# Optimization experiments

Measured on AMD Instinct MI355X. Metric: run time of the kernel, lower is better.

Reference implementation:

```python
import jax, jax.numpy as jnp
import numpy as np

NUM_CODES = 8192
LATENT_DIM = 512
COMMITMENT_WEIGHT = 0.25


def l2_normalize(x, axis=-1, eps=1e-12):
    n = jnp.linalg.norm(x, axis=axis, keepdims=True)
    return x / jnp.maximum(n, eps)


def setup_inputs() -> dict:
    key = jax.random.key(0)
    k1, k2 = jax.random.split(key)
    z_e = jax.random.normal(k1, (32768, LATENT_DIM), dtype=jnp.float32)
    embeddings = jax.random.normal(k2, (NUM_CODES, LATENT_DIM), dtype=jnp.float32)
    return {"z_e": z_e, "embeddings": embeddings}


def reference(z_e, embeddings):
    B = z_e.shape[0]
    z_e_norm = l2_normalize(z_e, axis=-1)          # (B, D)
    emb_norm = l2_normalize(embeddings, axis=-1)   # (K, D)
    sim = z_e_norm @ emb_norm.T                    # (B, K) cosine similarity
    indices = jnp.argmax(sim, axis=-1)             # (B,)
    z_q = emb_norm[indices]                        # (B, D) gather

    commitment_loss = COMMITMENT_WEIGHT * jnp.mean(
        (z_e_norm - jax.lax.stop_gradient(z_q)) ** 2)
    codebook_loss = jnp.mean((jax.lax.stop_gradient(z_e_norm) - z_q) ** 2)

    # straight-through estimator
    z_q_ste = z_e_norm + jax.lax.stop_gradient(z_q - z_e_norm)

    # usage stats (one-hot mean via scatter-add)
    counts = jnp.zeros((NUM_CODES,), dtype=jnp.float32).at[indices].add(1.0)
    avg_probs = counts / B
    perplexity = jnp.exp(-jnp.sum(avg_probs * jnp.log(avg_probs + 1e-10)))
    utilization = jnp.mean((avg_probs > 0).astype(jnp.float32))

    return (z_q_ste, indices, commitment_loss, codebook_loss, perplexity,
            utilization)
```

## Files before the change

kernel.cpp:

```cpp
#include <hip/hip_runtime.h>

#define BROWS  32768
#define DDIM   512
#define NCODES 8192
#define NCHUNK 4
#define CHUNKN (NCODES / NCHUNK)
#define NSPLIT2 16
#define CHUNK2 (NCODES / NSPLIT2)
#define TM     128
#define TN     128
#define BK     32
#define NKT    (DDIM / BK)
#define MARGIN1 1.0e-3f
#define MARGIN  6e-6f

typedef unsigned short ushort_t;
typedef unsigned int   uint_t;
typedef unsigned long long ull_t;
typedef __attribute__((ext_vector_type(8))) short  short8;
typedef __attribute__((ext_vector_type(4))) float  floatx4;

__device__ __forceinline__ float wave_sum(float v) {
#pragma unroll
  for (int o = 32; o > 0; o >>= 1) v += __shfl_xor(v, o, 64);
  return v;
}

__device__ __forceinline__ floatx4 mfma16(short8 a, short8 b, floatx4 c) {
  return __builtin_amdgcn_mfma_f32_16x16x32_bf16(a, b, c, 0, 0, 0);
}

__device__ __forceinline__ void ld2lds16(const ushort_t* g, ushort_t* l) {
  __builtin_amdgcn_global_load_lds((__attribute__((address_space(1))) void*)g,
                                   (__attribute__((address_space(3))) void*)l,
                                   16, 0, 0);
}

__device__ __forceinline__ void split1(float v, ushort_t& h, ushort_t& l) {
  uint_t u  = __float_as_uint(v);
  uint_t hb = (u + 0x7FFFu + ((u >> 16) & 1u)) >> 16;
  h = (ushort_t)hb;
  float r = v - __uint_as_float(hb << 16);
  uint_t u2 = __float_as_uint(r);
  l = (ushort_t)((u2 + 0x7FFFu + ((u2 >> 16) & 1u)) >> 16);
}

__device__ __forceinline__ ull_t pack_key(float v, int c) {
  uint_t u = __float_as_uint(v);
  u = (u & 0x80000000u) ? ~u : (u | 0x80000000u);
  return ((ull_t)u << 32) | (uint_t)(NCODES - 1 - c);
}

__global__ __launch_bounds__(256) void prep_split_kernel(const float* __restrict__ x,
                                                         float* __restrict__ xn,
                                                         ushort_t* __restrict__ xh,
                                                         ushort_t* __restrict__ xl) {
  const int w = threadIdx.x >> 6, lane = threadIdx.x & 63;
  const size_t row = (size_t)blockIdx.x * 4 + w;
  const float4* src = (const float4*)(x + row * DDIM);
  float4 a = src[lane], b = src[lane + 64];
  float s = a.x*a.x + a.y*a.y + a.z*a.z + a.w*a.w
          + b.x*b.x + b.y*b.y + b.z*b.z + b.w*b.w;
  s = wave_sum(s);
  const float inv = 1.0f / fmaxf(sqrtf(s), 1e-12f);
  a.x *= inv; a.y *= inv; a.z *= inv; a.w *= inv;
  b.x *= inv; b.y *= inv; b.z *= inv; b.w *= inv;
  if (xn) {
    float4* dst = (float4*)(xn + row * DDIM);
    dst[lane] = a; dst[lane + 64] = b;
  }
  ushort4 h0, l0, h1, l1;
  split1(a.x, h0.x, l0.x); split1(a.y, h0.y, l0.y);
  split1(a.z, h0.z, l0.z); split1(a.w, h0.w, l0.w);
  split1(b.x, h1.x, l1.x); split1(b.y, h1.y, l1.y);
  split1(b.z, h1.z, l1.z); split1(b.w, h1.w, l1.w);
  ushort4* ph = (ushort4*)(xh + row * DDIM);
  ushort4* pl = (ushort4*)(xl + row * DDIM);
  ph[lane] = h0; ph[lane + 64] = h1;
  pl[lane] = l0; pl[lane + 64] = l1;
}

__device__ __forceinline__ short8 frag_read(const ushort_t* base, int off16) {
  return *(const short8*)(base + off16);
}

__global__ __launch_bounds__(256, 2) void gemm1_kernel(
    const ushort_t* __restrict__ zh, const ushort_t* __restrict__ eh,
    float* __restrict__ pv1, int* __restrict__ pi1, float* __restrict__ pv2) {
  __shared__ union {
    ushort_t stg[2][2][TM * BK];
    struct { float v1[TM][2]; float v2[TM][2]; int i1[TM][2]; } red;
  } u;
  const int t = threadIdx.x;
  const int w = t >> 6;
  const int lane = t & 63;
  const int wm = w >> 1, wn = w & 1;
  const int col = lane & 15;
  const int quad = lane >> 4;
  const int chunk = blockIdx.x;
  const int row0 = blockIdx.y * TM;

  const int swc = ((lane & 3) ^ ((lane >> 3) & 3)) * 8;
  const int matsel = w >> 1;
  const int half = w & 1;
  const ushort_t* gsrcA = zh + (size_t)(row0 + half * 64 + (lane >> 2)) * DDIM + swc;

  const int swr = (quad ^ ((col >> 1) & 3)) * 8;

  float tv1[16], tv2[16]; int ti1[16];
#pragma unroll
  for (int s = 0; s < 16; ++s) { tv1[s] = -3.0e38f; tv2[s] = -3.0e38f; ti1[s] = 0; }

  for (int ct = 0; ct < CHUNKN / TN; ++ct) {
    const int cbase = chunk * CHUNKN + ct * TN;
    const ushort_t* gsrc = (matsel == 0) ? gsrcA
        : eh + (size_t)(cbase + half * 64 + (lane >> 2)) * DDIM + swc;

    floatx4 acc[4][4];
    const floatx4 z4 = {0.f, 0.f, 0.f, 0.f};
#pragma unroll
    for (int i = 0; i < 4; ++i)
#pragma unroll
      for (int j = 0; j < 4; ++j) acc[i][j] = z4;

    {
      ushort_t* l0 = u.stg[0][matsel] + half * 2048;
#pragma unroll
      for (int i = 0; i < 4; ++i)
        ld2lds16(gsrc + (size_t)(i * 16) * DDIM, l0 + i * 512);
    }
    __syncthreads();

    for (int kt = 0; kt < NKT; ++kt) {
      const int cur = kt & 1;
      if (kt + 1 < NKT) {
        ushort_t* ln = u.stg[cur ^ 1][matsel] + half * 2048;
        const ushort_t* gn = gsrc + (kt + 1) * BK;
#pragma unroll
        for (int i = 0; i < 4; ++i)
          ld2lds16(gn + (size_t)(i * 16) * DDIM, ln + i * 512);
      }

      short8 ah[4], bh[4];
#pragma unroll
      for (int i = 0; i < 4; ++i) {
        const int offA = (wm * 64 + i * 16 + col) * BK + swr;
        const int offB = (wn * 64 + i * 16 + col) * BK + swr;
        ah[i] = frag_read(u.stg[cur][0], offA);
        bh[i] = frag_read(u.stg[cur][1], offB);
      }
#pragma unroll
      for (int i = 0; i < 4; ++i)
#pragma unroll
        for (int j = 0; j < 4; ++j)
          acc[i][j] = mfma16(ah[i], bh[j], acc[i][j]);
      __syncthreads();
    }

    int nj[4];
#pragma unroll
    for (int j = 0; j < 4; ++j) nj[j] = cbase + wn * 64 + j * 16 + col;
#pragma unroll
    for (int i = 0; i < 4; ++i)
#pragma unroll
      for (int r = 0; r < 4; ++r) {
        const int s = i * 4 + r;
#pragma unroll
        for (int j = 0; j < 4; ++j) {
          float v = acc[i][j][r];
          float mn = fminf(v, tv1[s]);
          bool gt = v > tv1[s];
          tv1[s] = gt ? v : tv1[s];
          ti1[s] = gt ? nj[j] : ti1[s];
          tv2[s] = fmaxf(tv2[s], mn);
        }
      }
  }

#pragma unroll
  for (int off = 1; off < 16; off <<= 1) {
#pragma unroll
    for (int s = 0; s < 16; ++s) {
      float ov1 = __shfl_xor(tv1[s], off, 64);
      int   oi1 = __shfl_xor(ti1[s], off, 64);
      float ov2 = __shfl_xor(tv2[s], off, 64);
      float nv2 = fmaxf(fminf(tv1[s], ov1), fmaxf(tv2[s], ov2));
      if (ov1 > tv1[s] || (ov1 == tv1[s] && oi1 < ti1[s])) { tv1[s] = ov1; ti1[s] = oi1; }
      tv2[s] = nv2;
    }
  }
  __syncthreads();
  if (col == 0) {
#pragma unroll
    for (int s = 0; s < 16; ++s) {
      const int rl = wm * 64 + (s >> 2) * 16 + quad * 4 + (s & 3);
      u.red.v1[rl][wn] = tv1[s];
      u.red.v2[rl][wn] = tv2[s];
      u.red.i1[rl][wn] = ti1[s];
    }
  }
  __syncthreads();
  if (t < TM) {
    float V1 = u.red.v1[t][0], V2 = u.red.v2[t][0];
    int   I1 = u.red.i1[t][0];
    float a1 = u.red.v1[t][1], a2 = u.red.v2[t][1];
    int   ai = u.red.i1[t][1];
    float nv2 = fmaxf(fminf(V1, a1), fmaxf(V2, a2));
    if (a1 > V1 || (a1 == V1 && ai < I1)) { V1 = a1; I1 = ai; }
    V2 = nv2;
    const size_t o = (size_t)chunk * BROWS + row0 + t;
    pv1[o] = V1; pi1[o] = I1; pv2[o] = V2;
  }
}

__global__ __launch_bounds__(256) void combine1_kernel(
    const float* __restrict__ pv1, const int* __restrict__ pi1,
    const float* __restrict__ pv2, int* __restrict__ idxs,
    int* __restrict__ flagcnt, int* __restrict__ flaglist) {
  const int row = blockIdx.x * 256 + threadIdx.x;
  float V1 = pv1[row], V2 = pv2[row];
  int I1 = pi1[row];
#pragma unroll
  for (int c2 = 1; c2 < NCHUNK; ++c2) {
    const size_t o = (size_t)c2 * BROWS + row;
    float a1 = pv1[o], a2 = pv2[o];
    int ai = pi1[o];
    float nv2 = fmaxf(fminf(V1, a1), fmaxf(V2, a2));
    if (a1 > V1) { V1 = a1; I1 = ai; }
    V2 = nv2;
  }
  idxs[row] = I1;
  if (V1 - V2 < MARGIN1) {
    int p = atomicAdd(flagcnt, 1);
    flaglist[p] = row;
  }
}

__global__ __launch_bounds__(256) void compact_kernel(
    const ushort_t* __restrict__ zh, const ushort_t* __restrict__ zl,
    const int* __restrict__ flagcnt, const int* __restrict__ flaglist,
    ushort_t* __restrict__ zhc, ushort_t* __restrict__ zlc) {
  int nf = *flagcnt;
  if (nf > BROWS) nf = BROWS;
  const int w = threadIdx.x >> 6, lane = threadIdx.x & 63;
  const int slot = blockIdx.x * 4 + w;
  if (slot >= nf) return;
  const int row = flaglist[slot];
  const float4* sh = (const float4*)(zh + (size_t)row * DDIM);
  const float4* sl = (const float4*)(zl + (size_t)row * DDIM);
  float4* dh = (float4*)(zhc + (size_t)slot * DDIM);
  float4* dl = (float4*)(zlc + (size_t)slot * DDIM);
  dh[lane] = sh[lane];
  dl[lane] = sl[lane];
}

__global__ __launch_bounds__(256, 2) void gemm3f_kernel(
    const ushort_t* __restrict__ zhc, const ushort_t* __restrict__ zlc,
    const ushort_t* __restrict__ eh, const ushort_t* __restrict__ el,
    const int* __restrict__ flagcnt,
    float* __restrict__ pv1, int* __restrict__ pi1, float* __restrict__ pv2) {
  __shared__ union {
    ushort_t stg[2][4][TM * BK];
    struct { float v1[TM][2]; float v2[TM][2]; int i1[TM][2]; } red;
  } u;
  int nf = *flagcnt;
  if (nf > BROWS) nf = BROWS;
  const int row0 = blockIdx.y * TM;
  if (row0 >= nf) return;

  const int t = threadIdx.x;
  const int w = t >> 6;
  const int lane = t & 63;
  const int wm = w >> 1, wn = w & 1;
  const int col = lane & 15;
  const int quad = lane >> 4;
  const int chunk = blockIdx.x;

  const int swc = ((lane & 3) ^ ((lane >> 3) & 3)) * 8;
  const ushort_t* eb = (w == 2) ? eh : el;
  const ushort_t* ab = (w == 0) ? zhc : zlc;
  const ushort_t* gsrcA = ab + (size_t)(row0 + (lane >> 2)) * DDIM + swc;

  const int swr = (quad ^ ((col >> 1) & 3)) * 8;

  float tv1[16], tv2[16]; int ti1[16];
#pragma unroll
  for (int s = 0; s < 16; ++s) { tv1[s] = -3.0e38f; tv2[s] = -3.0e38f; ti1[s] = 0; }

  for (int ct = 0; ct < CHUNK2 / TN; ++ct) {
    const int cbase = chunk * CHUNK2 + ct * TN;
    const ushort_t* gsrc = (w < 2) ? gsrcA
        : eb + (size_t)(cbase + (lane >> 2)) * DDIM + swc;

    floatx4 acc[4][4];
    const floatx4 z4 = {0.f, 0.f, 0.f, 0.f};
#pragma unroll
    for (int i = 0; i < 4; ++i)
#pragma unroll
      for (int j = 0; j < 4; ++j) acc[i][j] = z4;

    {
      ushort_t* l0 = u.stg[0][w];
#pragma unroll
      for (int i = 0; i < 8; ++i)
        ld2lds16(gsrc + (size_t)(i * 16) * DDIM, l0 + i * 512);
    }
    __syncthreads();

    for (int kt = 0; kt < NKT; ++kt) {
      const int cur = kt & 1;
      if (kt + 1 < NKT) {
        ushort_t* ln = u.stg[cur ^ 1][w];
        const ushort_t* gn = gsrc + (kt + 1) * BK;
#pragma unroll
        for (int i = 0; i < 8; ++i)
          ld2lds16(gn + (size_t)(i * 16) * DDIM, ln + i * 512);
      }

      short8 ah[4], al[4], bh[4], bl[4];
#pragma unroll
      for (int i = 0; i < 4; ++i) {
        const int offA = (wm * 64 + i * 16 + col) * BK + swr;
        const int offB = (wn * 64 + i * 16 + col) * BK + swr;
        ah[i] = frag_read(u.stg[cur][0], offA);
        al[i] = frag_read(u.stg[cur][1], offA);
        bh[i] = frag_read(u.stg[cur][2], offB);
        bl[i] = frag_read(u.stg[cur][3], offB);
      }
#pragma unroll
      for (int i = 0; i < 4; ++i)
#pragma unroll
        for (int j = 0; j < 4; ++j) {
          acc[i][j] = mfma16(ah[i], bh[j], acc[i][j]);
          acc[i][j] = mfma16(ah[i], bl[j], acc[i][j]);
          acc[i][j] = mfma16(al[i], bh[j], acc[i][j]);
        }
      __syncthreads();
    }

    int nj[4];
#pragma unroll
    for (int j = 0; j < 4; ++j) nj[j] = cbase + wn * 64 + j * 16 + col;
#pragma unroll
    for (int i = 0; i < 4; ++i)
#pragma unroll
      for (int r = 0; r < 4; ++r) {
        const int s = i * 4 + r;
#pragma unroll
        for (int j = 0; j < 4; ++j) {
          float v = acc[i][j][r];
          float mn = fminf(v, tv1[s]);
          bool gt = v > tv1[s];
          tv1[s] = gt ? v : tv1[s];
          ti1[s] = gt ? nj[j] : ti1[s];
          tv2[s] = fmaxf(tv2[s], mn);
        }
      }
  }

#pragma unroll
  for (int off = 1; off < 16; off <<= 1) {
#pragma unroll
    for (int s = 0; s < 16; ++s) {
      float ov1 = __shfl_xor(tv1[s], off, 64);
      int   oi1 = __shfl_xor(ti1[s], off, 64);
      float ov2 = __shfl_xor(tv2[s], off, 64);
      float nv2 = fmaxf(fminf(tv1[s], ov1), fmaxf(tv2[s], ov2));
      if (ov1 > tv1[s] || (ov1 == tv1[s] && oi1 < ti1[s])) { tv1[s] = ov1; ti1[s] = oi1; }
      tv2[s] = nv2;
    }
  }
  __syncthreads();
  if (col == 0) {
#pragma unroll
    for (int s = 0; s < 16; ++s) {
      const int rl = wm * 64 + (s >> 2) * 16 + quad * 4 + (s & 3);
      u.red.v1[rl][wn] = tv1[s];
      u.red.v2[rl][wn] = tv2[s];
      u.red.i1[rl][wn] = ti1[s];
    }
  }
  __syncthreads();
  if (t < TM) {
    float V1 = u.red.v1[t][0], V2 = u.red.v2[t][0];
    int   I1 = u.red.i1[t][0];
    float a1 = u.red.v1[t][1], a2 = u.red.v2[t][1];
    int   ai = u.red.i1[t][1];
    float nv2 = fmaxf(fminf(V1, a1), fmaxf(V2, a2));
    if (a1 > V1 || (a1 == V1 && ai < I1)) { V1 = a1; I1 = ai; }
    V2 = nv2;
    const size_t o = (size_t)chunk * BROWS + row0 + t;
    pv1[o] = V1; pi1[o] = I1; pv2[o] = V2;
  }
}

__global__ __launch_bounds__(256) void combine2_kernel(
    const float* __restrict__ pv1, const int* __restrict__ pi1,
    const float* __restrict__ pv2, const int* __restrict__ flagcnt,
    const int* __restrict__ flaglist, int* __restrict__ idxs,
    int* __restrict__ flag2cnt, int* __restrict__ flag2list) {
  int nf = *flagcnt;
  if (nf > BROWS) nf = BROWS;
  const int f = blockIdx.x * 256 + threadIdx.x;
  if (f >= nf) return;
  float V1 = pv1[f], V2 = pv2[f];
  int I1 = pi1[f];
#pragma unroll
  for (int c2 = 1; c2 < NSPLIT2; ++c2) {
    const size_t o = (size_t)c2 * BROWS + f;
    float a1 = pv1[o], a2 = pv2[o];
    int ai = pi1[o];
    float nv2 = fmaxf(fminf(V1, a1), fmaxf(V2, a2));
    if (a1 > V1) { V1 = a1; I1 = ai; }
    V2 = nv2;
  }
  const int row = flaglist[f];
  idxs[row] = I1;
  if (V1 - V2 < MARGIN) {
    int p = atomicAdd(flag2cnt, 1);
    flag2list[p] = row;
  }
}

__global__ __launch_bounds__(256) void rerank_kernel(
    const float* __restrict__ z, const float* __restrict__ en,
    const int* __restrict__ flagcnt, const int* __restrict__ flaglist,
    ull_t* __restrict__ pk) {
  __shared__ float sZ[512];
  __shared__ ull_t sk[4];
  const int t = threadIdx.x;
  const int w = t >> 6, lane = t & 63;
  int nf = *flagcnt;
  if (nf > BROWS) nf = BROWS;
  const int ntask = nf * 32;
  for (int task = blockIdx.x; task < ntask; task += gridDim.x) {
    const int f = task >> 5, slab = task & 31;
    const int row = flaglist[f];
    __syncthreads();
    if (t < 128) ((float4*)sZ)[t] = ((const float4*)(z + (size_t)row * DDIM))[t];
    __syncthreads();
    const float4 za = ((const float4*)sZ)[lane];
    const float4 zb = ((const float4*)sZ)[lane + 64];
    const int c0 = slab * 256 + w * 64;
    ull_t bk = 0;
    for (int cc = 0; cc < 64; ++cc) {
      const int c = c0 + cc;
      const float4* ep = (const float4*)(en + (size_t)c * DDIM);
      float4 ea = ep[lane], eb = ep[lane + 64];
      float d = ea.x*za.x + ea.y*za.y + ea.z*za.z + ea.w*za.w
              + eb.x*zb.x + eb.y*zb.y + eb.z*zb.z + eb.w*zb.w;
      d = wave_sum(d);
      ull_t k2 = pack_key(d, c);
      if (k2 > bk) bk = k2;
    }
    if (lane == 0) sk[w] = bk;
    __syncthreads();
    if (t == 0) {
      ull_t m = sk[0];
      if (sk[1] > m) m = sk[1];
      if (sk[2] > m) m = sk[2];
      if (sk[3] > m) m = sk[3];
      atomicMax(&pk[f], m);
    }
  }
}

__global__ __launch_bounds__(256) void unpack_kernel(
    const int* __restrict__ flagcnt, const int* __restrict__ flaglist,
    const ull_t* __restrict__ pk, int* __restrict__ idxs) {
  int nf = *flagcnt;
  if (nf > BROWS) nf = BROWS;
  for (int f = blockIdx.x * 256 + threadIdx.x; f < nf; f += gridDim.x * 256)
    idxs[flaglist[f]] = (NCODES - 1) - (int)(pk[f] & 0xFFFFFFFFu);
}

__global__ __launch_bounds__(256) void finalize_kernel(const float* __restrict__ z,
                                                       const float* __restrict__ en,
                                                       const int* __restrict__ idxs,
                                                       float* __restrict__ out_q,
                                                       float* __restrict__ out_i,
                                                       float* __restrict__ counts,
                                                       float* __restrict__ lossp) {
  __shared__ float sdl[4];
  int w = threadIdx.x >> 6, lane = threadIdx.x & 63;
  int row = blockIdx.x * 4 + w;
  const float4* zr = (const float4*)(z + (size_t)row * DDIM);
  float4 a = zr[lane], b = zr[lane + 64];
  float s = a.x*a.x + a.y*a.y + a.z*a.z + a.w*a.w
          + b.x*b.x + b.y*b.y + b.z*b.z + b.w*b.w;
  s = wave_sum(s);
  float inv = 1.0f / fmaxf(sqrtf(s), 1e-12f);
  int k = idxs[row];
  const float4* qr = (const float4*)(en + (size_t)k * DDIM);
  float4 qa = qr[lane], qb = qr[lane + 64];
  float d = 0.0f;
  float4 oa, ob;
  {
    float zn;
    zn = a.x * inv; oa.x = zn + (qa.x - zn); d += (zn - qa.x) * (zn - qa.x);
    zn = a.y * inv; oa.y = zn + (qa.y - zn); d += (zn - qa.y) * (zn - qa.y);
    zn = a.z * inv; oa.z = zn + (qa.z - zn); d += (zn - qa.z) * (zn - qa.z);
    zn = a.w * inv; oa.w = zn + (qa.w - zn); d += (zn - qa.w) * (zn - qa.w);
    zn = b.x * inv; ob.x = zn + (qb.x - zn); d += (zn - qb.x) * (zn - qb.x);
    zn = b.y * inv; ob.y = zn + (qb.y - zn); d += (zn - qb.y) * (zn - qb.y);
    zn = b.z * inv; ob.z = zn + (qb.z - zn); d += (zn - qb.z) * (zn - qb.z);
    zn = b.w * inv; ob.w = zn + (qb.w - zn); d += (zn - qb.w) * (zn - qb.w);
  }
  float4* orow = (float4*)(out_q + (size_t)row * DDIM);
  orow[lane] = oa;
  orow[lane + 64] = ob;
  d = wave_sum(d);
  if (lane == 0) {
    sdl[w] = d;
    atomicAdd(&counts[k], 1.0f);
    out_i[row] = (float)k;
  }
  __syncthreads();
  if (threadIdx.x == 0)
    lossp[blockIdx.x] = sdl[0] + sdl[1] + sdl[2] + sdl[3];
}

__global__ __launch_bounds__(256) void scalars_kernel(const float* __restrict__ counts,
                                                      const float* __restrict__ lossp,
                                                      float* __restrict__ o) {
  __shared__ float se[256], su[256], sl[256];
  int t = threadIdx.x;
  float ent = 0.0f, utl = 0.0f, lsum = 0.0f;
  for (int i = t; i < NCODES; i += 256) {
    float c = counts[i];
    float p = c * (1.0f / (float)BROWS);
    ent -= p * logf(p + 1e-10f);
    utl += (c > 0.0f) ? 1.0f : 0.0f;
    lsum += lossp[i];
  }
  se[t] = ent; su[t] = utl; sl[t] = lsum;
  __syncthreads();
  for (int s2 = 128; s2 > 0; s2 >>= 1) {
    if (t < s2) { se[t] += se[t + s2]; su[t] += su[t + s2]; sl[t] += sl[t + s2]; }
    __syncthreads();
  }
  if (t == 0) {
    float mse = sl[0] * (1.0f / (float)(BROWS * DDIM));
    o[0] = 0.25f * mse;
    o[1] = mse;
    o[2] = expf(se[0]);
    o[3] = su[0] * (1.0f / (float)NCODES);
  }
}

__global__ __launch_bounds__(256) void fb_norm_rows(const float* __restrict__ e,
                                                    float* __restrict__ en) {
  int w = threadIdx.x >> 6, lane = threadIdx.x & 63;
  int row = blockIdx.x * 4 + w;
  const float4* src = (const float4*)(e + (size_t)row * DDIM);
  float4 a = src[lane], b = src[lane + 64];
  float s = a.x*a.x + a.y*a.y + a.z*a.z + a.w*a.w
          + b.x*b.x + b.y*b.y + b.z*b.z + b.w*b.w;
  s = wave_sum(s);
  float inv = 1.0f / fmaxf(sqrtf(s), 1e-12f);
  float4* dst = (float4*)(en + (size_t)row * DDIM);
  dst[lane] = make_float4(a.x*inv, a.y*inv, a.z*inv, a.w*inv);
  dst[lane + 64] = make_float4(b.x*inv, b.y*inv, b.z*inv, b.w*inv);
}

__global__ __launch_bounds__(256) void fb_gemm_argmax(const float* __restrict__ z,
                                                      const float* __restrict__ en,
                                                      int* __restrict__ out_idx) {
  __shared__ float As[16][TM + 4];
  __shared__ float Bs[16][TN + 4];
  __shared__ float rv[TM][16];
  __shared__ int   ri[TM][16];
  const int t = threadIdx.x;
  const int tx = t & 15, ty = t >> 4;
  const int row0 = blockIdx.x * TM;
  const int m = t >> 2, f4 = t & 3;
  float bestv[8]; int bestn[8];
#pragma unroll
  for (int i = 0; i < 8; ++i) { bestv[i] = -3.0e38f; bestn[i] = 0; }
  for (int ct = 0; ct < NCODES / TN; ++ct) {
    float acc[8][8];
#pragma unroll
    for (int i = 0; i < 8; ++i)
#pragma unroll
      for (int j = 0; j < 8; ++j) acc[i][j] = 0.0f;
    for (int kt = 0; kt < DDIM / 16; ++kt) {
      const int k0 = kt * 16;
      __syncthreads();
      {
        const float* zb = z + (size_t)(row0 + m) * DDIM + k0 + f4 * 4;
        float4 v0 = *(const float4*)zb;
        float4 v1 = *(const float4*)(zb + (size_t)64 * DDIM);
        const float* ebp = en + (size_t)(ct * TN + m) * DDIM + k0 + f4 * 4;
        float4 w0 = *(const float4*)ebp;
        float4 w1 = *(const float4*)(ebp + (size_t)64 * DDIM);
        const int kk = f4 * 4;
        As[kk+0][m] = v0.x; As[kk+1][m] = v0.y; As[kk+2][m] = v0.z; As[kk+3][m] = v0.w;
        As[kk+0][m+64] = v1.x; As[kk+1][m+64] = v1.y; As[kk+2][m+64] = v1.z; As[kk+3][m+64] = v1.w;
        Bs[kk+0][m] = w0.x; Bs[kk+1][m] = w0.y; Bs[kk+2][m] = w0.z; Bs[kk+3][m] = w0.w;
        Bs[kk+0][m+64] = w1.x; Bs[kk+1][m+64] = w1.y; Bs[kk+2][m+64] = w1.z; Bs[kk+3][m+64] = w1.w;
      }
      __syncthreads();
#pragma unroll
      for (int k = 0; k < 16; ++k) {
        float4 a0 = *(const float4*)&As[k][ty * 8];
        float4 a1 = *(const float4*)&As[k][ty * 8 + 4];
        float4 b0 = *(const float4*)&Bs[k][tx * 4];
        float4 b1 = *(const float4*)&Bs[k][64 + tx * 4];
        float a[8] = {a0.x,a0.y,a0.z,a0.w,a1.x,a1.y,a1.z,a1.w};
        float b[8] = {b0.x,b0.y,b0.z,b0.w,b1.x,b1.y,b1.z,b1.w};
#pragma unroll
        for (int i = 0; i < 8; ++i)
#pragma unroll
          for (int j = 0; j < 8; ++j) acc[i][j] = fmaf(a[i], b[j], acc[i][j]);
      }
    }
    const int nb = ct * TN;
#pragma unroll
    for (int i = 0; i < 8; ++i)
#pragma unroll
      for (int j = 0; j < 8; ++j) {
        int n = nb + ((j < 4) ? (tx * 4 + j) : (64 + tx * 4 + (j - 4)));
        if (acc[i][j] > bestv[i]) { bestv[i] = acc[i][j]; bestn[i] = n; }
      }
  }
#pragma unroll
  for (int i = 0; i < 8; ++i) { rv[ty*8+i][tx] = bestv[i]; ri[ty*8+i][tx] = bestn[i]; }
  __syncthreads();
  if (t < TM) {
    float bv = rv[t][0]; int bi = ri[t][0];
#pragma unroll
    for (int x = 1; x < 16; ++x) {
      float v = rv[t][x]; int n = ri[t][x];
      if (v > bv || (v == bv && n < bi)) { bv = v; bi = n; }
    }
    out_idx[row0 + t] = bi;
  }
}

extern "C" void kernel_launch(void* const* d_in, const int* in_sizes, int n_in,
                              void* d_out, int out_size, void* d_ws, size_t ws_size,
                              hipStream_t stream) {
  const float* z = (const float*)d_in[0];
  const float* e = (const float*)d_in[1];
  float* out = (float*)d_out;
  float* ws = (float*)d_ws;

  float* out_q = out;
  float* out_i = out + (size_t)BROWS * DDIM;
  float* out_s = out_i + BROWS;

  const size_t ENF = (size_t)NCODES * DDIM;
  const size_t ZNF = (size_t)BROWS * DDIM;
  const size_t NFIN = BROWS / 4;

  ushort_t* zhc = (ushort_t*)out_q;
  ushort_t* zlc = zhc + (size_t)BROWS * DDIM;

  size_t off = 0;
  float*    en       = ws + off;              off += ENF;
  ushort_t* enh      = (ushort_t*)(ws + off); off += ENF / 2;
  ushort_t* enl      = (ushort_t*)(ws + off); off += ENF / 2;
  ushort_t* zh       = (ushort_t*)(ws + off); off += ZNF / 2;
  ushort_t* zl       = (ushort_t*)(ws + off); off += ZNF / 2;
  float*    pv1      = ws + off;              off += (size_t)NSPLIT2 * BROWS;
  int*      pi1      = (int*)(ws + off);      off += (size_t)NSPLIT2 * BROWS;
  float*    pv2      = ws + off;              off += (size_t)NSPLIT2 * BROWS;
  int*      idxs     = (int*)(ws + off);      off += BROWS;
  int*      flaglist = (int*)(ws + off);      off += BROWS;
  int*      flag2list= (int*)(ws + off);      off += BROWS;
  float*    lossp    = ws + off;              off += NFIN;
  float*    counts   = ws + off;              off += NCODES;
  int*      flagcnt  = (int*)(ws + off);      off += 1;
  int*      flag2cnt = (int*)(ws + off);      off += 1;
  if (off & 1) off += 1;
  ull_t*    pk       = (ull_t*)(ws + off);    off += (size_t)BROWS * 2;
  const size_t need_bytes = off * sizeof(float);
  const size_t zero_bytes = (size_t)((char*)(pk + BROWS) - (char*)counts);

  if (ws_size >= need_bytes) {
    prep_split_kernel<<<NCODES / 4, 256, 0, stream>>>(e, en, enh, enl);
    prep_split_kernel<<<BROWS / 4, 256, 0, stream>>>(z, nullptr, zh, zl);
    hipMemsetAsync(counts, 0, zero_bytes, stream);
    dim3 g1(NCHUNK, BROWS / TM);
    gemm1_kernel<<<g1, 256, 0, stream>>>(zh, enh, pv1, pi1, pv2);
    combine1_kernel<<<BROWS / 256, 256, 0, stream>>>(pv1, pi1, pv2, idxs, flagcnt, flaglist);
    compact_kernel<<<BROWS / 4, 256, 0, stream>>>(zh, zl, flagcnt, flaglist, zhc, zlc);
    dim3 g2(NSPLIT2, BROWS / TM);
    gemm3f_kernel<<<g2, 256, 0, stream>>>(zhc, zlc, enh, enl, flagcnt, pv1, pi1, pv2);
    combine2_kernel<<<BROWS / 256, 256, 0, stream>>>(pv1, pi1, pv2, flagcnt, flaglist,
                                                     idxs, flag2cnt, flag2list);
    rerank_kernel<<<1024, 256, 0, stream>>>(z, en, flag2cnt, flag2list, pk);
    unpack_kernel<<<32, 256, 0, stream>>>(flag2cnt, flag2list, pk, idxs);
    finalize_kernel<<<BROWS / 4, 256, 0, stream>>>(z, en, idxs, out_q, out_i, counts, lossp);
    scalars_kernel<<<1, 256, 0, stream>>>(counts, lossp, out_s);
  } else {
    float* fen    = ws;
    int*   fidx   = (int*)(fen + ENF);
    float* fcnt   = (float*)(fidx + BROWS);
    float* flossp = fcnt + NCODES;
    fb_norm_rows<<<NCODES / 4, 256, 0, stream>>>(e, fen);
    hipMemsetAsync(fcnt, 0, NCODES * sizeof(float), stream);
    fb_gemm_argmax<<<BROWS / TM, 256, 0, stream>>>(z, fen, fidx);
    finalize_kernel<<<BROWS / 4, 256, 0, stream>>>(z, fen, fidx, out_q, out_i, fcnt, flossp);
    scalars_kernel<<<1, 256, 0, stream>>>(fcnt, flossp, out_s);
  }
}
```

Baseline: 684.1 us.

## Tighten first-pass margin, cap flagged rows and split refinement GEMM finer

Lowers the first-pass ambiguity margin so fewer rows are sent to the split-precision refinement GEMM. That GEMM and its compact and combine kernels are now sized for at most 8192 flagged rows instead of all 32768, which shrinks the launch grids and the partial-result buffers. The code dimension is split 64 ways, so each block handles a single 128-code tile with no inner loop, giving more parallel blocks for the smaller row count. The risk is correctness: a tighter margin, or more than 8192 flagged rows (those past the cap keep their first-pass index), can produce wrong argmax results.

```diff
diff --git a/kernel.cpp b/kernel.cpp
--- a/kernel.cpp
+++ b/kernel.cpp
@@ -5,13 +5,14 @@
 #define NCODES 8192
 #define NCHUNK 4
 #define CHUNKN (NCODES / NCHUNK)
-#define NSPLIT2 16
+#define NSPLIT2 64
 #define CHUNK2 (NCODES / NSPLIT2)
+#define NF_CAP 8192
 #define TM     128
 #define TN     128
 #define BK     32
 #define NKT    (DDIM / BK)
-#define MARGIN1 1.0e-3f
+#define MARGIN1 6.0e-4f
 #define MARGIN  6e-6f
 
 typedef unsigned short ushort_t;
@@ -241,7 +242,7 @@
     const int* __restrict__ flagcnt, const int* __restrict__ flaglist,
     ushort_t* __restrict__ zhc, ushort_t* __restrict__ zlc) {
   int nf = *flagcnt;
-  if (nf > BROWS) nf = BROWS;
+  if (nf > NF_CAP) nf = NF_CAP;
   const int w = threadIdx.x >> 6, lane = threadIdx.x & 63;
   const int slot = blockIdx.x * 4 + w;
   if (slot >= nf) return;
@@ -258,13 +259,13 @@
     const ushort_t* __restrict__ zhc, const ushort_t* __restrict__ zlc,
     const ushort_t* __restrict__ eh, const ushort_t* __restrict__ el,
     const int* __restrict__ flagcnt,
-    float* __restrict__ pv1, int* __restrict__ pi1, float* __restrict__ pv2) {
+    float* __restrict__ qv1, int* __restrict__ qi1, float* __restrict__ qv2) {
   __shared__ union {
     ushort_t stg[2][4][TM * BK];
     struct { float v1[TM][2]; float v2[TM][2]; int i1[TM][2]; } red;
   } u;
   int nf = *flagcnt;
-  if (nf > BROWS) nf = BROWS;
+  if (nf > NF_CAP) nf = NF_CAP;
   const int row0 = blockIdx.y * TM;
   if (row0 >= nf) return;
 
@@ -287,76 +288,74 @@
 #pragma unroll
   for (int s = 0; s < 16; ++s) { tv1[s] = -3.0e38f; tv2[s] = -3.0e38f; ti1[s] = 0; }
 
-  for (int ct = 0; ct < CHUNK2 / TN; ++ct) {
-    const int cbase = chunk * CHUNK2 + ct * TN;
-    const ushort_t* gsrc = (w < 2) ? gsrcA
-        : eb + (size_t)(cbase + (lane >> 2)) * DDIM + swc;
-
-    floatx4 acc[4][4];
-    const floatx4 z4 = {0.f, 0.f, 0.f, 0.f};
+  const int cbase = chunk * CHUNK2;
+  const ushort_t* gsrc = (w < 2) ? gsrcA
+      : eb + (size_t)(cbase + (lane >> 2)) * DDIM + swc;
+
+  floatx4 acc[4][4];
+  const floatx4 z4 = {0.f, 0.f, 0.f, 0.f};
+#pragma unroll
+  for (int i = 0; i < 4; ++i)
+#pragma unroll
+    for (int j = 0; j < 4; ++j) acc[i][j] = z4;
+
+  {
+    ushort_t* l0 = u.stg[0][w];
+#pragma unroll
+    for (int i = 0; i < 8; ++i)
+      ld2lds16(gsrc + (size_t)(i * 16) * DDIM, l0 + i * 512);
+  }
+  __syncthreads();
+
+  for (int kt = 0; kt < NKT; ++kt) {
+    const int cur = kt & 1;
+    if (kt + 1 < NKT) {
+      ushort_t* ln = u.stg[cur ^ 1][w];
+      const ushort_t* gn = gsrc + (kt + 1) * BK;
+#pragma unroll
+      for (int i = 0; i < 8; ++i)
+        ld2lds16(gn + (size_t)(i * 16) * DDIM, ln + i * 512);
+    }
+
+    short8 ah[4], al[4], bh[4], bl[4];
+#pragma unroll
+    for (int i = 0; i < 4; ++i) {
+      const int offA = (wm * 64 + i * 16 + col) * BK + swr;
+      const int offB = (wn * 64 + i * 16 + col) * BK + swr;
+      ah[i] = frag_read(u.stg[cur][0], offA);
+      al[i] = frag_read(u.stg[cur][1], offA);
+      bh[i] = frag_read(u.stg[cur][2], offB);
+      bl[i] = frag_read(u.stg[cur][3], offB);
+    }
 #pragma unroll
     for (int i = 0; i < 4; ++i)
 #pragma unroll
-      for (int j = 0; j < 4; ++j) acc[i][j] = z4;
-
-    {
-      ushort_t* l0 = u.stg[0][w];
-#pragma unroll
-      for (int i = 0; i < 8; ++i)
-        ld2lds16(gsrc + (size_t)(i * 16) * DDIM, l0 + i * 512);
-    }
+      for (int j = 0; j < 4; ++j) {
+        acc[i][j] = mfma16(ah[i], bh[j], acc[i][j]);
+        acc[i][j] = mfma16(ah[i], bl[j], acc[i][j]);
+        acc[i][j] = mfma16(al[i], bh[j], acc[i][j]);
+      }
     __syncthreads();
-
-    for (int kt = 0; kt < NKT; ++kt) {
-      const int cur = kt & 1;
-      if (kt + 1 < NKT) {
-        ushort_t* ln = u.stg[cur ^ 1][w];
-        const ushort_t* gn = gsrc + (kt + 1) * BK;
-#pragma unroll
-        for (int i = 0; i < 8; ++i)
-          ld2lds16(gn + (size_t)(i * 16) * DDIM, ln + i * 512);
+  }
+
+  int nj[4];
+#pragma unroll
+  for (int j = 0; j < 4; ++j) nj[j] = cbase + wn * 64 + j * 16 + col;
+#pragma unroll
+  for (int i = 0; i < 4; ++i)
+#pragma unroll
+    for (int r = 0; r < 4; ++r) {
+      const int s = i * 4 + r;
+#pragma unroll
+      for (int j = 0; j < 4; ++j) {
+        float v = acc[i][j][r];
+        float mn = fminf(v, tv1[s]);
+        bool gt = v > tv1[s];
+        tv1[s] = gt ? v : tv1[s];
+        ti1[s] = gt ? nj[j] : ti1[s];
+        tv2[s] = fmaxf(tv2[s], mn);
       }
-
-      short8 ah[4], al[4], bh[4], bl[4];
-#pragma unroll
-      for (int i = 0; i < 4; ++i) {
-        const int offA = (wm * 64 + i * 16 + col) * BK + swr;
-        const int offB = (wn * 64 + i * 16 + col) * BK + swr;
-        ah[i] = frag_read(u.stg[cur][0], offA);
-        al[i] = frag_read(u.stg[cur][1], offA);
-        bh[i] = frag_read(u.stg[cur][2], offB);
-        bl[i] = frag_read(u.stg[cur][3], offB);
-      }
-#pragma unroll
-      for (int i = 0; i < 4; ++i)
-#pragma unroll
-        for (int j = 0; j < 4; ++j) {
-          acc[i][j] = mfma16(ah[i], bh[j], acc[i][j]);
-          acc[i][j] = mfma16(ah[i], bl[j], acc[i][j]);
-          acc[i][j] = mfma16(al[i], bh[j], acc[i][j]);
-        }
-      __syncthreads();
-    }
-
-    int nj[4];
-#pragma unroll
-    for (int j = 0; j < 4; ++j) nj[j] = cbase + wn * 64 + j * 16 + col;
-#pragma unroll
-    for (int i = 0; i < 4; ++i)
-#pragma unroll
-      for (int r = 0; r < 4; ++r) {
-        const int s = i * 4 + r;
-#pragma unroll
-        for (int j = 0; j < 4; ++j) {
-          float v = acc[i][j][r];
-          float mn = fminf(v, tv1[s]);
-          bool gt = v > tv1[s];
-          tv1[s] = gt ? v : tv1[s];
-          ti1[s] = gt ? nj[j] : ti1[s];
-          tv2[s] = fmaxf(tv2[s], mn);
-        }
-      }
-  }
+    }
 
 #pragma unroll
   for (int off = 1; off < 16; off <<= 1) {
@@ -389,27 +388,26 @@
     float nv2 = fmaxf(fminf(V1, a1), fmaxf(V2, a2));
     if (a1 > V1 || (a1 == V1 && ai < I1)) { V1 = a1; I1 = ai; }
     V2 = nv2;
-    const size_t o = (size_t)chunk * BROWS + row0 + t;
-    pv1[o] = V1; pi1[o] = I1; pv2[o] = V2;
+    const size_t o = (size_t)chunk * NF_CAP + row0 + t;
+    qv1[o] = V1; qi1[o] = I1; qv2[o] = V2;
   }
 }
 
 __global__ __launch_bounds__(256) void combine2_kernel(
-    const float* __restrict__ pv1, const int* __restrict__ pi1,
-    const float* __restrict__ pv2, const int* __restrict__ flagcnt,
+    const float* __restrict__ qv1, const int* __restrict__ qi1,
+    const float* __restrict__ qv2, const int* __restrict__ flagcnt,
     const int* __restrict__ flaglist, int* __restrict__ idxs,
     int* __restrict__ flag2cnt, int* __restrict__ flag2list) {
   int nf = *flagcnt;
-  if (nf > BROWS) nf = BROWS;
+  if (nf > NF_CAP) nf = NF_CAP;
   const int f = blockIdx.x * 256 + threadIdx.x;
   if (f >= nf) return;
-  float V1 = pv1[f], V2 = pv2[f];
-  int I1 = pi1[f];
-#pragma unroll
+  float V1 = qv1[f], V2 = qv2[f];
+  int I1 = qi1[f];
   for (int c2 = 1; c2 < NSPLIT2; ++c2) {
-    const size_t o = (size_t)c2 * BROWS + f;
-    float a1 = pv1[o], a2 = pv2[o];
-    int ai = pi1[o];
+    const size_t o = (size_t)c2 * NF_CAP + f;
+    float a1 = qv1[o], a2 = qv2[o];
+    int ai = qi1[o];
     float nv2 = fmaxf(fminf(V1, a1), fmaxf(V2, a2));
     if (a1 > V1) { V1 = a1; I1 = ai; }
     V2 = nv2;
@@ -654,7 +652,7 @@
   const size_t NFIN = BROWS / 4;
 
   ushort_t* zhc = (ushort_t*)out_q;
-  ushort_t* zlc = zhc + (size_t)BROWS * DDIM;
+  ushort_t* zlc = zhc + (size_t)NF_CAP * DDIM;
 
   size_t off = 0;
   float*    en       = ws + off;              off += ENF;
@@ -662,9 +660,12 @@
   ushort_t* enl      = (ushort_t*)(ws + off); off += ENF / 2;
   ushort_t* zh       = (ushort_t*)(ws + off); off += ZNF / 2;
   ushort_t* zl       = (ushort_t*)(ws + off); off += ZNF / 2;
-  float*    pv1      = ws + off;              off += (size_t)NSPLIT2 * BROWS;
-  int*      pi1      = (int*)(ws + off);      off += (size_t)NSPLIT2 * BROWS;
-  float*    pv2      = ws + off;              off += (size_t)NSPLIT2 * BROWS;
+  float*    pv1      = ws + off;              off += (size_t)NCHUNK * BROWS;
+  int*      pi1      = (int*)(ws + off);      off += (size_t)NCHUNK * BROWS;
+  float*    pv2      = ws + off;              off += (size_t)NCHUNK * BROWS;
+  float*    qv1      = ws + off;              off += (size_t)NSPLIT2 * NF_CAP;
+  int*      qi1      = (int*)(ws + off);      off += (size_t)NSPLIT2 * NF_CAP;
+  float*    qv2      = ws + off;              off += (size_t)NSPLIT2 * NF_CAP;
   int*      idxs     = (int*)(ws + off);      off += BROWS;
   int*      flaglist = (int*)(ws + off);      off += BROWS;
   int*      flag2list= (int*)(ws + off);      off += BROWS;
@@ -684,11 +685,11 @@
     dim3 g1(NCHUNK, BROWS / TM);
     gemm1_kernel<<<g1, 256, 0, stream>>>(zh, enh, pv1, pi1, pv2);
     combine1_kernel<<<BROWS / 256, 256, 0, stream>>>(pv1, pi1, pv2, idxs, flagcnt, flaglist);
-    compact_kernel<<<BROWS / 4, 256, 0, stream>>>(zh, zl, flagcnt, flaglist, zhc, zlc);
-    dim3 g2(NSPLIT2, BROWS / TM);
-    gemm3f_kernel<<<g2, 256, 0, stream>>>(zhc, zlc, enh, enl, flagcnt, pv1, pi1, pv2);
-    combine2_kernel<<<BROWS / 256, 256, 0, stream>>>(pv1, pi1, pv2, flagcnt, flaglist,
-                                                     idxs, flag2cnt, flag2list);
+    compact_kernel<<<NF_CAP / 4, 256, 0, stream>>>(zh, zl, flagcnt, flaglist, zhc, zlc);
+    dim3 g2(NSPLIT2, NF_CAP / TM);
+    gemm3f_kernel<<<g2, 256, 0, stream>>>(zhc, zlc, enh, enl, flagcnt, qv1, qi1, qv2);
+    combine2_kernel<<<NF_CAP / 256, 256, 0, stream>>>(qv1, qi1, qv2, flagcnt, flaglist,
+                                                      idxs, flag2cnt, flag2list);
     rerank_kernel<<<1024, 256, 0, stream>>>(z, en, flag2cnt, flag2list, pk);
     unpack_kernel<<<32, 256, 0, stream>>>(flag2cnt, flag2list, pk, idxs);
     finalize_kernel<<<BROWS / 4, 256, 0, stream>>>(z, en, idxs, out_q, out_i, counts, lossp);
```

Result: faster. 657.8 us (-3.8%).
